# Kernel optimization log

Hardware: AMD Instinct MI355X
Metric: run time of the kernel (lower is better)

Reference implementation:

```python
import jax, jax.numpy as jnp
import numpy as np

M = 48      # number of MPS components / Fourier modes
L = 48      # num_site
N = 256     # batch of samples
PI = float(np.pi)


def setup_inputs() -> dict:
    key = jax.random.key(0)
    k1, k2, k3, k4 = jax.random.split(key, 4)
    inp = jax.random.uniform(k1, (N, L), jnp.float32)
    theta = 0.01 * jax.random.uniform(k2, (L, M), jnp.float32, minval=-PI / 2, maxval=PI / 2)
    coef = 1.0 + 0.01 * jax.random.uniform(k3, (M,), jnp.float32, minval=-1.0, maxval=1.0)
    rand_u = jax.random.uniform(k4, (L, N), jnp.float32)
    return {"inp": inp, "theta": theta, "coef": coef, "rand_u": rand_u}


def _output_mps(inp, theta, coef):
    # fourier encoding: angle (N,M,L) = inp (N,L) * m*pi/2
    m_vals = jnp.arange(1, M + 1, dtype=inp.dtype)
    angle = inp[:, None, :] * (m_vals * (PI / 2))[None, :, None]
    emb = jnp.stack([jnp.cos(angle), jnp.sin(angle)], axis=-1)  # (N,M,L,2)
    c, s = jnp.cos(theta), jnp.sin(theta)                        # (L,M)
    R = jnp.stack([jnp.stack([c, -s], axis=-1), jnp.stack([s, c], axis=-1)], axis=-2)  # (L,M,2,2)
    mpo = jnp.transpose(R, (1, 0, 2, 3))                         # (M,L,2,2)
    return jnp.einsum('m,mlpq,nmlq->nmlp', coef, mpo, emb)       # (N,M,L,2)


def _inner(mps):
    # vmapped inner_product: sum_{m,k} prod_l <mps[m,l], mps[k,l]>
    t = jnp.einsum('nmlp,nklp->nmkl', mps, mps)  # (N,M,M,L)
    return jnp.sum(jnp.prod(t, axis=-1), axis=(1, 2))  # (N,)


def _zipper(mps, rand_u):
    # Incremental form of zipper_MPS: zeroing the (1-bit) component at each
    # re-cloning + re-masking the full prefix every step (same math).
    e0 = jnp.array([1.0, 0.0], mps.dtype)  # zeroes component 0 (bit=1 branch)
    e1 = jnp.array([0.0, 1.0], mps.dtype)  # zeroes component 1 (bit=0 branch)
    pos = jnp.arange(L)

    def step(mps_cur, xs):
        l, u = xs
        oh = (pos == l).astype(mps_cur.dtype)                     # (L,) one-hot at site l
        denom = jnp.abs(_inner(mps_cur))                           # marginal_prob(prefix)
        mps1 = mps_cur * (1.0 - oh[None, None, :, None] * e0)     # assume bit=1 at l
        p1 = jnp.abs(_inner(mps1)) / denom
        bit = (u < p1).astype(jnp.int32)                           # (N,)
        mps0 = mps_cur * (1.0 - oh[None, None, :, None] * e1)     # bit=0 branch
        mps_new = jnp.where((bit == 1)[:, None, None, None], mps1, mps0)
        return mps_new, bit

    mps_final, bits = jax.lax.scan(step, mps, (pos, rand_u))
    measurement = bits.T                                           # (N,L) int32
    P_m = jnp.abs(_inner(mps_final)) / jnp.abs(_inner(mps))        # normalized prob
    return measurement, P_m


def reference(inp, theta, coef, rand_u):
    mps = _output_mps(inp, theta, coef)
    return _zipper(mps, rand_u)
```

## Files before the change

### kernel.cpp

```cpp
#include <hip/hip_runtime.h>
#include <math.h>

#define M_ 48
#define L_ 48
#define N_ 256
#define THREADS 512
#define NWAVE 8
#define PPT 3

struct ChunkTab { short cm[THREADS]; short ck0[THREADS]; };
constexpr ChunkTab make_tab() {
    ChunkTab t{};
    int bsz[16] = {};
    for (int m = 0; m < 48; ++m)
        for (int j = 0; PPT * j < 48 - m; ++j) bsz[(m + PPT * j) & 15]++;
    int slot = 0;
    for (int r = 0; r < 64; ++r)
        for (int b = 0; b < 16; ++b)
            if (bsz[b] > r) {
                int cnt = 0;
                for (int m = 0; m < 48; ++m)
                    for (int j = 0; PPT * j < 48 - m; ++j)
                        if (((m + PPT * j) & 15) == b) {
                            if (cnt == r) { t.cm[slot] = (short)m; t.ck0[slot] = (short)(m + PPT * j); }
                            ++cnt;
                        }
                ++slot;
            }
    for (; slot < THREADS; ++slot) { t.cm[slot] = 0; t.ck0[slot] = 127; }
    return t;
}
__device__ constexpr ChunkTab g_tab = make_tab();

template<int CTRL, int RMASK>
__device__ __forceinline__ double dpp_add(double v) {
    int lo = __builtin_amdgcn_update_dpp(0, __double2loint(v), CTRL, RMASK, 0xf, true);
    int hi = __builtin_amdgcn_update_dpp(0, __double2hiint(v), CTRL, RMASK, 0xf, true);
    return v + __hiloint2double(hi, lo);
}
__device__ __forceinline__ double wave_sum63(double v) {
    v = dpp_add<0x111, 0xf>(v);
    v = dpp_add<0x112, 0xf>(v);
    v = dpp_add<0x114, 0xf>(v);
    v = dpp_add<0x118, 0xf>(v);
    v = dpp_add<0x142, 0xa>(v);
    v = dpp_add<0x143, 0xc>(v);
    return v;
}

__launch_bounds__(THREADS, 2)
__global__ void mps_sample_kernel(const float* __restrict__ inp,
                                  const float* __restrict__ theta,
                                  const float* __restrict__ coef,
                                  const float* __restrict__ rand_u,
                                  float* __restrict__ out)
{
    const int n   = blockIdx.x;
    const int tid = threadIdx.x;

    __shared__ float  s_pxy[L_][M_][2];
    __shared__ double s_part[2][4][NWAVE];
    __shared__ float  s_u[L_];

    const double PI_2 = 1.5707963267948966;

    #pragma unroll
    for (int i = 0; i < 5; ++i) {
        int j = tid + THREADS * i;
        if (j < L_ * M_) {
            int l = j / M_, m = j - l * M_;
            double a  = (double)inp[n * L_ + l] * ((double)(m + 1) * PI_2);
            double th = (double)theta[l * M_ + m];
            double sv, cv; sincos(th + a, &sv, &cv);
            double cf = (double)coef[m];
            s_pxy[l][m][0] = (float)(cf * cv);
            s_pxy[l][m][1] = (float)(cf * sv);
        }
    }
    if (tid < L_) s_u[tid] = rand_u[tid * N_ + n];

    const int cm = g_tab.cm[tid];
    const int k0 = g_tab.ck0[tid];
    int pk[PPT]; double wgt[PPT];
    #pragma unroll
    for (int i = 0; i < PPT; ++i) {
        int k = k0 + i;
        wgt[i] = (k > 47) ? 0.0 : ((k == cm) ? 1.0 : 2.0);
        pk[i]  = (k > 47) ? 47 : k;
    }
    __syncthreads();

    double ckpt[5][PPT];
    {
        double C[PPT];
        #pragma unroll
        for (int i = 0; i < PPT; ++i) C[i] = wgt[i];
        #pragma unroll
        for (int s = 4; s >= 0; --s) {
            #pragma unroll
            for (int lp = 7; lp >= 0; --lp) {
                int l = 8 * (s + 1) + lp;
                float2 vm = *(const float2*)&s_pxy[l][cm][0];
                #pragma unroll
                for (int i = 0; i < PPT; ++i) {
                    float2 vk = *(const float2*)&s_pxy[l][pk[i]][0];
                    C[i] *= (double)fmaf(vm.x, vk.x, vm.y * vk.y);
                }
            }
            #pragma unroll
            for (int i = 0; i < PPT; ++i) ckpt[s][i] = C[i];
        }
    }

    double G[PPT];
    #pragma unroll
    for (int i = 0; i < PPT; ++i) G[i] = 1.0;

    double denom = 0.0, initd = 1.0;
    float  myBit = 0.0f;

    #pragma unroll
    for (int seg = 0; seg < 6; ++seg) {
        double T[8][PPT];
        #pragma unroll
        for (int j = 0; j < 8; ++j) {
            int l2 = 8 * seg + j;
            float2 vm = *(const float2*)&s_pxy[l2][cm][0];
            #pragma unroll
            for (int i = 0; i < PPT; ++i) {
                float2 vk = *(const float2*)&s_pxy[l2][pk[i]][0];
                T[j][i] = (double)(vm.x * vk.x) + (double)(vm.y * vk.y);
            }
        }
        double R[8][PPT];
        #pragma unroll
        for (int i = 0; i < PPT; ++i)
            R[7][i] = (seg == 5) ? wgt[i] : ckpt[seg == 5 ? 0 : seg][i];
        #pragma unroll
        for (int j = 6; j >= 0; --j)
            #pragma unroll
            for (int i = 0; i < PPT; ++i)
                R[j][i] = R[j + 1][i] * T[j + 1][i];

        #pragma unroll
        for (int half = 0; half < 4; ++half) {
            const int ls  = 2 * half;
            const int l   = 8 * seg + ls;
            const int par = half & 1;
            float2 vm0 = *(const float2*)&s_pxy[l][cm][0];
            float2 vm1 = *(const float2*)&s_pxy[l + 1][cm][0];
            double X0[PPT], Y0[PPT], X1[PPT], Y1[PPT];
            #pragma unroll
            for (int i = 0; i < PPT; ++i) {
                float2 vk0 = *(const float2*)&s_pxy[l][pk[i]][0];
                float2 vk1 = *(const float2*)&s_pxy[l + 1][pk[i]][0];
                X0[i] = (double)(vm0.x * vk0.x);
                Y0[i] = (double)(vm0.y * vk0.y);
                X1[i] = (double)(vm1.x * vk1.x);
                Y1[i] = (double)(vm1.y * vk1.y);
            }
            double n1L = 0.0, h0 = 0.0, h1 = 0.0, nT = 0.0;
            #pragma unroll
            for (int i = 0; i < PPT; ++i) {
                double t0 = G[i] * R[ls][i];
                double t1 = G[i] * R[ls + 1][i];
                n1L = fma(t0, Y0[i], n1L);
                if (seg == 0 && half == 0) nT = fma(t0, X0[i], nT);
                h0 = fma(t1 * X0[i], Y1[i], h0);
                h1 = fma(t1 * Y0[i], Y1[i], h1);
            }
            n1L = wave_sum63(n1L);
            h0  = wave_sum63(h0);
            h1  = wave_sum63(h1);
            if (seg == 0 && half == 0) nT = wave_sum63(nT);
            if ((tid & 63) == 63) {
                const int wv = tid >> 6;
                s_part[par][0][wv] = n1L; s_part[par][1][wv] = h0;
                s_part[par][2][wv] = h1;
                if (seg == 0 && half == 0) s_part[par][3][wv] = nT;
            }
            __syncthreads();
            double2 a0 = *(const double2*)&s_part[par][0][0];
            double2 b0 = *(const double2*)&s_part[par][0][2];
            double2 c0v = *(const double2*)&s_part[par][0][4];
            double2 d0v = *(const double2*)&s_part[par][0][6];
            double2 a1 = *(const double2*)&s_part[par][1][0];
            double2 b1 = *(const double2*)&s_part[par][1][2];
            double2 c1v = *(const double2*)&s_part[par][1][4];
            double2 d1v = *(const double2*)&s_part[par][1][6];
            double2 a2 = *(const double2*)&s_part[par][2][0];
            double2 b2 = *(const double2*)&s_part[par][2][2];
            double2 c2v = *(const double2*)&s_part[par][2][4];
            double2 d2v = *(const double2*)&s_part[par][2][6];
            double sn1 = ((a0.x + a0.y) + (b0.x + b0.y)) + ((c0v.x + c0v.y) + (d0v.x + d0v.y));
            double sh0 = ((a1.x + a1.y) + (b1.x + b1.y)) + ((c1v.x + c1v.y) + (d1v.x + d1v.y));
            double sh1 = ((a2.x + a2.y) + (b2.x + b2.y)) + ((c2v.x + c2v.y) + (d2v.x + d2v.y));
            if (seg == 0 && half == 0) {
                double2 a3 = *(const double2*)&s_part[par][3][0];
                double2 b3 = *(const double2*)&s_part[par][3][2];
                double2 c3v = *(const double2*)&s_part[par][3][4];
                double2 d3v = *(const double2*)&s_part[par][3][6];
                double snT = ((a3.x + a3.y) + (b3.x + b3.y)) + ((c3v.x + c3v.y) + (d3v.x + d3v.y));
                denom = fabs(snT + sn1);
                initd = denom;
            }
            double v1 = fabs(sn1);
            int bitA   = ((double)s_u[l] * denom < v1) ? 1 : 0;
            denom      = bitA ? v1 : fabs(denom - sn1);
            double n1b = bitA ? sh1 : sh0;
            double v2  = fabs(n1b);
            int bitB   = ((double)s_u[l + 1] * denom < v2) ? 1 : 0;
            denom      = bitB ? v2 : fabs(denom - n1b);
            #pragma unroll
            for (int i = 0; i < PPT; ++i) {
                double c0 = bitA ? Y0[i] : X0[i];
                double c1 = bitB ? Y1[i] : X1[i];
                G[i] *= c0 * c1;
            }
            if (tid == l)     myBit = (float)bitA;
            if (tid == l + 1) myBit = (float)bitB;
        }
    }

    if (tid < L_)  out[n * L_ + tid] = myBit;
    if (tid == 0)  out[N_ * L_ + n] = (float)(denom / initd);
}

extern "C" void kernel_launch(void* const* d_in, const int* in_sizes, int n_in,
                              void* d_out, int out_size, void* d_ws, size_t ws_size,
                              hipStream_t stream) {
    const float* inp    = (const float*)d_in[0];
    const float* theta  = (const float*)d_in[1];
    const float* coef   = (const float*)d_in[2];
    const float* rand_u = (const float*)d_in[3];
    float* out = (float*)d_out;
    mps_sample_kernel<<<N_, THREADS, 0, stream>>>(inp, theta, coef, rand_u, out);
}
```

Before: 84.78 us.

## Resolve four sequential site measurements per barrier via speculative branch sums

Each block-wide reduction round now covers four consecutive sites instead of two. It computes partial sums for every possible combination of earlier bits in the group (1+2+4+8 sums) and then picks the right one once the bits are known. This halves the number of __syncthreads barriers and reduction rounds per segment. In exchange it does more FP64 arithmetic, 15 wave reductions instead of 3 per round, and uses more registers and shared memory, which could hurt occupancy.

```diff
diff --git a/kernel.cpp b/kernel.cpp
--- a/kernel.cpp
+++ b/kernel.cpp
@@ -59,7 +59,7 @@
     const int tid = threadIdx.x;
 
     __shared__ float  s_pxy[L_][M_][2];
-    __shared__ double s_part[2][4][NWAVE];
+    __shared__ double s_part[2][16][NWAVE];
     __shared__ float  s_u[L_];
 
     const double PI_2 = 1.5707963267948966;
@@ -143,82 +143,137 @@
                 R[j][i] = R[j + 1][i] * T[j + 1][i];
 
         #pragma unroll
-        for (int half = 0; half < 4; ++half) {
-            const int ls  = 2 * half;
-            const int l   = 8 * seg + ls;
-            const int par = half & 1;
+        for (int halfq = 0; halfq < 2; ++halfq) {
+            const int ls    = 4 * halfq;
+            const int l     = 8 * seg + ls;
+            const int par   = halfq;
+            const bool first = (seg == 0 && halfq == 0);
             float2 vm0 = *(const float2*)&s_pxy[l][cm][0];
             float2 vm1 = *(const float2*)&s_pxy[l + 1][cm][0];
+            float2 vm2 = *(const float2*)&s_pxy[l + 2][cm][0];
+            float2 vm3 = *(const float2*)&s_pxy[l + 3][cm][0];
             double X0[PPT], Y0[PPT], X1[PPT], Y1[PPT];
+            double X2[PPT], Y2[PPT], X3[PPT], Y3[PPT];
             #pragma unroll
             for (int i = 0; i < PPT; ++i) {
                 float2 vk0 = *(const float2*)&s_pxy[l][pk[i]][0];
                 float2 vk1 = *(const float2*)&s_pxy[l + 1][pk[i]][0];
-                X0[i] = (double)(vm0.x * vk0.x);
-                Y0[i] = (double)(vm0.y * vk0.y);
-                X1[i] = (double)(vm1.x * vk1.x);
-                Y1[i] = (double)(vm1.y * vk1.y);
-            }
-            double n1L = 0.0, h0 = 0.0, h1 = 0.0, nT = 0.0;
+                float2 vk2 = *(const float2*)&s_pxy[l + 2][pk[i]][0];
+                float2 vk3 = *(const float2*)&s_pxy[l + 3][pk[i]][0];
+                X0[i] = (double)(vm0.x * vk0.x);  Y0[i] = (double)(vm0.y * vk0.y);
+                X1[i] = (double)(vm1.x * vk1.x);  Y1[i] = (double)(vm1.y * vk1.y);
+                X2[i] = (double)(vm2.x * vk2.x);  Y2[i] = (double)(vm2.y * vk2.y);
+                X3[i] = (double)(vm3.x * vk3.x);  Y3[i] = (double)(vm3.y * vk3.y);
+            }
+            double n1 = 0.0, nT = 0.0;
+            double h0 = 0.0, h1 = 0.0;
+            double hh00 = 0.0, hh01 = 0.0, hh10 = 0.0, hh11 = 0.0;
+            double k000 = 0.0, k001 = 0.0, k010 = 0.0, k011 = 0.0;
+            double k100 = 0.0, k101 = 0.0, k110 = 0.0, k111 = 0.0;
             #pragma unroll
             for (int i = 0; i < PPT; ++i) {
                 double t0 = G[i] * R[ls][i];
                 double t1 = G[i] * R[ls + 1][i];
-                n1L = fma(t0, Y0[i], n1L);
-                if (seg == 0 && half == 0) nT = fma(t0, X0[i], nT);
-                h0 = fma(t1 * X0[i], Y1[i], h0);
-                h1 = fma(t1 * Y0[i], Y1[i], h1);
-            }
-            n1L = wave_sum63(n1L);
-            h0  = wave_sum63(h0);
-            h1  = wave_sum63(h1);
-            if (seg == 0 && half == 0) nT = wave_sum63(nT);
+                double t2 = G[i] * R[ls + 2][i];
+                double t3 = G[i] * R[ls + 3][i];
+                n1 = fma(t0, Y0[i], n1);
+                if (first) nT = fma(t0, X0[i], nT);
+                double a0 = t1 * X0[i], a1 = t1 * Y0[i];
+                h0 = fma(a0, Y1[i], h0);
+                h1 = fma(a1, Y1[i], h1);
+                double b0 = t2 * X0[i], b1 = t2 * Y0[i];
+                double b00 = b0 * X1[i], b01 = b0 * Y1[i];
+                double b10 = b1 * X1[i], b11 = b1 * Y1[i];
+                hh00 = fma(b00, Y2[i], hh00);
+                hh01 = fma(b01, Y2[i], hh01);
+                hh10 = fma(b10, Y2[i], hh10);
+                hh11 = fma(b11, Y2[i], hh11);
+                double e0 = t3 * X0[i], e1 = t3 * Y0[i];
+                double e00 = e0 * X1[i], e01 = e0 * Y1[i];
+                double e10 = e1 * X1[i], e11 = e1 * Y1[i];
+                k000 = fma(e00 * X2[i], Y3[i], k000);
+                k001 = fma(e00 * Y2[i], Y3[i], k001);
+                k010 = fma(e01 * X2[i], Y3[i], k010);
+                k011 = fma(e01 * Y2[i], Y3[i], k011);
+                k100 = fma(e10 * X2[i], Y3[i], k100);
+                k101 = fma(e10 * Y2[i], Y3[i], k101);
+                k110 = fma(e11 * X2[i], Y3[i], k110);
+                k111 = fma(e11 * Y2[i], Y3[i], k111);
+            }
+            n1   = wave_sum63(n1);
+            h0   = wave_sum63(h0);   h1   = wave_sum63(h1);
+            hh00 = wave_sum63(hh00); hh01 = wave_sum63(hh01);
+            hh10 = wave_sum63(hh10); hh11 = wave_sum63(hh11);
+            k000 = wave_sum63(k000); k001 = wave_sum63(k001);
+            k010 = wave_sum63(k010); k011 = wave_sum63(k011);
+            k100 = wave_sum63(k100); k101 = wave_sum63(k101);
+            k110 = wave_sum63(k110); k111 = wave_sum63(k111);
+            if (first) nT = wave_sum63(nT);
             if ((tid & 63) == 63) {
                 const int wv = tid >> 6;
-                s_part[par][0][wv] = n1L; s_part[par][1][wv] = h0;
-                s_part[par][2][wv] = h1;
-                if (seg == 0 && half == 0) s_part[par][3][wv] = nT;
+                s_part[par][0][wv]  = n1;
+                s_part[par][1][wv]  = h0;   s_part[par][2][wv]  = h1;
+                s_part[par][3][wv]  = hh00; s_part[par][4][wv]  = hh01;
+                s_part[par][5][wv]  = hh10; s_part[par][6][wv]  = hh11;
+                s_part[par][7][wv]  = k000; s_part[par][8][wv]  = k001;
+                s_part[par][9][wv]  = k010; s_part[par][10][wv] = k011;
+                s_part[par][11][wv] = k100; s_part[par][12][wv] = k101;
+                s_part[par][13][wv] = k110; s_part[par][14][wv] = k111;
+                if (first) s_part[par][15][wv] = nT;
             }
             __syncthreads();
-            double2 a0 = *(const double2*)&s_part[par][0][0];
-            double2 b0 = *(const double2*)&s_part[par][0][2];
-            double2 c0v = *(const double2*)&s_part[par][0][4];
-            double2 d0v = *(const double2*)&s_part[par][0][6];
-            double2 a1 = *(const double2*)&s_part[par][1][0];
-            double2 b1 = *(const double2*)&s_part[par][1][2];
-            double2 c1v = *(const double2*)&s_part[par][1][4];
-            double2 d1v = *(const double2*)&s_part[par][1][6];
-            double2 a2 = *(const double2*)&s_part[par][2][0];
-            double2 b2 = *(const double2*)&s_part[par][2][2];
-            double2 c2v = *(const double2*)&s_part[par][2][4];
-            double2 d2v = *(const double2*)&s_part[par][2][6];
-            double sn1 = ((a0.x + a0.y) + (b0.x + b0.y)) + ((c0v.x + c0v.y) + (d0v.x + d0v.y));
-            double sh0 = ((a1.x + a1.y) + (b1.x + b1.y)) + ((c1v.x + c1v.y) + (d1v.x + d1v.y));
-            double sh1 = ((a2.x + a2.y) + (b2.x + b2.y)) + ((c2v.x + c2v.y) + (d2v.x + d2v.y));
-            if (seg == 0 && half == 0) {
-                double2 a3 = *(const double2*)&s_part[par][3][0];
-                double2 b3 = *(const double2*)&s_part[par][3][2];
-                double2 c3v = *(const double2*)&s_part[par][3][4];
-                double2 d3v = *(const double2*)&s_part[par][3][6];
-                double snT = ((a3.x + a3.y) + (b3.x + b3.y)) + ((c3v.x + c3v.y) + (d3v.x + d3v.y));
-                denom = fabs(snT + sn1);
+            auto rd8 = [&](int v) -> double {
+                double2 a = *(const double2*)&s_part[par][v][0];
+                double2 b = *(const double2*)&s_part[par][v][2];
+                double2 c = *(const double2*)&s_part[par][v][4];
+                double2 d = *(const double2*)&s_part[par][v][6];
+                return ((a.x + a.y) + (b.x + b.y)) + ((c.x + c.y) + (d.x + d.y));
+            };
+            double S_n1   = rd8(0);
+            double S_h0   = rd8(1),  S_h1   = rd8(2);
+            double S_hh00 = rd8(3),  S_hh01 = rd8(4);
+            double S_hh10 = rd8(5),  S_hh11 = rd8(6);
+            double S_k000 = rd8(7),  S_k001 = rd8(8);
+            double S_k010 = rd8(9),  S_k011 = rd8(10);
+            double S_k100 = rd8(11), S_k101 = rd8(12);
+            double S_k110 = rd8(13), S_k111 = rd8(14);
+            if (first) {
+                double snT = rd8(15);
+                denom = fabs(snT + S_n1);
                 initd = denom;
             }
-            double v1 = fabs(sn1);
-            int bitA   = ((double)s_u[l] * denom < v1) ? 1 : 0;
-            denom      = bitA ? v1 : fabs(denom - sn1);
-            double n1b = bitA ? sh1 : sh0;
-            double v2  = fabs(n1b);
-            int bitB   = ((double)s_u[l + 1] * denom < v2) ? 1 : 0;
-            denom      = bitB ? v2 : fabs(denom - n1b);
-            #pragma unroll
-            for (int i = 0; i < PPT; ++i) {
-                double c0 = bitA ? Y0[i] : X0[i];
-                double c1 = bitB ? Y1[i] : X1[i];
-                G[i] *= c0 * c1;
+            double v1 = fabs(S_n1);
+            int bitA  = ((double)s_u[l] * denom < v1) ? 1 : 0;
+            denom     = bitA ? v1 : fabs(denom - S_n1);
+            double nB = bitA ? S_h1 : S_h0;
+            double v2 = fabs(nB);
+            int bitB  = ((double)s_u[l + 1] * denom < v2) ? 1 : 0;
+            denom     = bitB ? v2 : fabs(denom - nB);
+            double nC = bitA ? (bitB ? S_hh11 : S_hh10)
+                             : (bitB ? S_hh01 : S_hh00);
+            double v3 = fabs(nC);
+            int bitC  = ((double)s_u[l + 2] * denom < v3) ? 1 : 0;
+            denom     = bitC ? v3 : fabs(denom - nC);
+            double nD0 = bitB ? (bitC ? S_k011 : S_k010)
+                              : (bitC ? S_k001 : S_k000);
+            double nD1 = bitB ? (bitC ? S_k111 : S_k110)
+                              : (bitC ? S_k101 : S_k100);
+            double nD = bitA ? nD1 : nD0;
+            double v4 = fabs(nD);
+            int bitD  = ((double)s_u[l + 3] * denom < v4) ? 1 : 0;
+            denom     = bitD ? v4 : fabs(denom - nD);
+            #pragma unroll
+            for (int i = 0; i < PPT; ++i) {
+                double f0 = bitA ? Y0[i] : X0[i];
+                double f1 = bitB ? Y1[i] : X1[i];
+                double f2 = bitC ? Y2[i] : X2[i];
+                double f3 = bitD ? Y3[i] : X3[i];
+                G[i] *= (f0 * f1) * (f2 * f3);
             }
             if (tid == l)     myBit = (float)bitA;
             if (tid == l + 1) myBit = (float)bitB;
+            if (tid == l + 2) myBit = (float)bitC;
+            if (tid == l + 3) myBit = (float)bitD;
         }
     }
 
```

After: 105.3 us. 24.2% more time.
